# Performance work log

Measured on AMD Instinct MI355X. Metric: run time of the kernel, lower is better.

Reference implementation:

```python
import jax, jax.numpy as jnp
import numpy as np

NUM_GRAPHS = 4
N_NODES = 50000
N_EDGES = 800000
D_IN = 64
D_HID = 64
D_OUT = 64


def setup_inputs() -> dict:
    key = jax.random.key(0)
    ks = jax.random.split(key, 8)
    x = jax.random.normal(ks[0], (NUM_GRAPHS, N_NODES, D_IN), dtype=jnp.float32)
    edge_index = jax.random.randint(ks[1], (NUM_GRAPHS, 2, N_EDGES), 0, N_NODES, dtype=jnp.int64)
    s = 0.05
    W_l1 = jax.random.normal(ks[2], (NUM_GRAPHS, D_IN, D_HID), dtype=jnp.float32) * s
    W_r1 = jax.random.normal(ks[3], (NUM_GRAPHS, D_IN, D_HID), dtype=jnp.float32) * s
    b1 = jax.random.normal(ks[4], (NUM_GRAPHS, D_HID), dtype=jnp.float32) * s
    W_l2 = jax.random.normal(ks[5], (NUM_GRAPHS, D_HID, D_OUT), dtype=jnp.float32) * s
    W_r2 = jax.random.normal(ks[6], (NUM_GRAPHS, D_HID, D_OUT), dtype=jnp.float32) * s
    b2 = jax.random.normal(ks[7], (NUM_GRAPHS, D_OUT), dtype=jnp.float32) * s
    return {"x": x, "edge_index": edge_index, "W_l1": W_l1, "W_r1": W_r1,
            "b1": b1, "W_l2": W_l2, "W_r2": W_r2, "b2": b2}


def _sage_conv(x, src, dst, W_l, W_r, b):
    # PyG SAGEConv (aggr='mean', root_weight=True): mean(x[src] -> dst) @ W_l + b + x @ W_r
    n = x.shape[0]
    msgs = x[src]                                            # [E, d] irregular gather
    agg = jax.ops.segment_sum(msgs, dst, num_segments=n)     # [N, d]
    deg = jax.ops.segment_sum(jnp.ones((src.shape[0],), x.dtype), dst, num_segments=n)
    mean = agg / jnp.maximum(deg, 1.0)[:, None]              # empty neighborhoods -> 0
    return mean @ W_l + b + x @ W_r


def _per_graph(x, edge_index, W_l1, W_r1, b1, W_l2, W_r2, b2):
    src, dst = edge_index[0], edge_index[1]
    h = jax.nn.elu(_sage_conv(x, src, dst, W_l1, W_r1, b1))
    return jax.nn.elu(_sage_conv(h, src, dst, W_l2, W_r2, b2))


def reference(x, edge_index, W_l1, W_r1, b1, W_l2, W_r2, b2):
    out = jax.vmap(_per_graph)(x, edge_index, W_l1, W_r1, b1, W_l2, W_r2, b2)  # [G, N, out]
    return out.reshape(-1, out.shape[-1])  # concat along node dim -> [G*N, out]
```

## Files before the change

kernel.cpp:

```cpp
#include <hip/hip_runtime.h>
#include <hip/hip_bf16.h>
#include <math.h>

#define NG 4
#define NN 50000
#define NE 800000
#define DD 64
#define CAP 64
#define NT 64
#define NTILE 391
#define NTG (2 * NTILE)
#define RCAP 1536
#define CPAD 16
#define PBLK 128
#define CHUNK (NE / PBLK)
#define LBINS 392
#define BCAP 20

typedef __attribute__((ext_vector_type(8))) short short8;
typedef __attribute__((ext_vector_type(4))) float float4v;

__device__ __forceinline__ unsigned short f2b(float f) {
    union { __hip_bfloat16 h; unsigned short u; } cv;
    cv.h = __float2bfloat16(f);
    return cv.u;
}
__device__ __forceinline__ float b2f(unsigned short u) {
    union { unsigned short u; __hip_bfloat16 h; } cv;
    cv.u = u;
    return __bfloat162float(cv.h);
}

__global__ void init_kernel(const int* __restrict__ ei, int* __restrict__ flags) {
    __shared__ alignas(16) unsigned short A[16 * 32];
    __shared__ unsigned short B[32 * 16];
    int t = threadIdx.x;
    int any_nonzero = 0;
    for (int i = t; i < 128; i += 64) any_nonzero |= ei[2 * i + 1];
    unsigned long long nz = __ballot(any_nonzero != 0);
    int is64 = (nz == 0ULL) ? 1 : 0;
    for (int i = t; i < 512; i += 64) {
        int r = i >> 5, k = i & 31;
        A[i] = f2b((float)(((r * 5 + k * 3) & 31) - 15));
        int kk = i >> 4, c = i & 15;
        B[i] = f2b((float)(((kk * 7 + c * 11) & 31) - 15));
    }
    __syncthreads();
    short8 a = *(const short8*)&A[(t & 15) * 32 + (t >> 4) * 8];
    int c = t & 15, kb = (t >> 4) * 8;
    short8 b;
    for (int j = 0; j < 8; ++j) b[j] = (short)B[(kb + j) * 16 + c];
    float4v acc = {0.f, 0.f, 0.f, 0.f};
    acc = __builtin_amdgcn_mfma_f32_16x16x32_bf16(a, b, acc, 0, 0, 0);
    int ok = 1;
    for (int reg = 0; reg < 4; ++reg) {
        int row = (t >> 4) * 4 + reg;
        float ref = 0.f;
        for (int k = 0; k < 32; ++k)
            ref += (float)(((row * 5 + k * 3) & 31) - 15) *
                   (float)(((k * 7 + c * 11) & 31) - 15);
        if (acc[reg] != ref) ok = 0;
    }
    unsigned long long vote = __ballot(ok);
    if (t == 0) flags[0] = is64 | ((vote == ~0ULL) ? 2 : 0);
}

__device__ __forceinline__ int nt_idx(const int* __restrict__ ei, long pos, int is64) {
    return is64 ? __builtin_nontemporal_load(ei + 2 * pos)
                : __builtin_nontemporal_load(ei + pos);
}

__global__ void partition_kernel(const int* __restrict__ ei, const int* __restrict__ flags,
                                 int* __restrict__ bcnt, unsigned int* __restrict__ part) {
    __shared__ int lcnt[LBINS];
    __shared__ int basev[LBINS];
    __shared__ unsigned int lbuf[LBINS * BCAP];

    int is64 = flags[0] & 1;
    int s = blockIdx.x & 7;
    int g = s >> 1;
    int lo = (s & 1) * (NN / 2), hi = lo + (NN / 2);
    int rbase0 = lo >> 6;
    int bsl = blockIdx.x >> 3;
    int e0 = bsl * CHUNK, e1 = e0 + CHUNK;
    long ebase = (long)g * 2 * NE;

    for (int i = threadIdx.x; i < LBINS; i += 256) lcnt[i] = 0;
    __syncthreads();

    for (int e = e0 + threadIdx.x; e < e1; e += 256) {
        int d = nt_idx(ei, ebase + NE + e, is64);
        int sc = nt_idx(ei, ebase + e, is64);
        if (d >= lo && d < hi) {
            int lb = (d >> 6) - rbase0;
            unsigned int pk = ((unsigned int)d << 16) | (unsigned int)(sc & 0xffff);
            int pos = atomicAdd(&lcnt[lb], 1);
            if (pos < BCAP) {
                lbuf[lb * BCAP + pos] = pk;
            } else {
                int gp = atomicAdd(&bcnt[(g * NTG + (d >> 6)) * CPAD], 1);
                if (gp < RCAP) part[(long)(g * NTG + (d >> 6)) * RCAP + gp] = pk;
            }
        }
    }
    __syncthreads();

    for (int r = threadIdx.x; r < LBINS; r += 256) {
        int c = lcnt[r]; c = c < BCAP ? c : BCAP;
        basev[r] = c ? atomicAdd(&bcnt[(g * NTG + rbase0 + r) * CPAD], c) : 0;
    }
    __syncthreads();

    int w = threadIdx.x >> 6, hw = (threadIdx.x >> 5) & 1, l32 = threadIdx.x & 31;
    for (int r = w * 2 + hw; r < LBINS; r += 8) {
        int c = lcnt[r]; c = c < BCAP ? c : BCAP;
        int b = basev[r];
        if (l32 < c && b + l32 < RCAP)
            part[(long)(g * NTG + rbase0 + r) * RCAP + b + l32] = lbuf[r * BCAP + l32];
    }
}

__global__ void convert_kernel(const float* __restrict__ x, unsigned short* __restrict__ xb) {
    long total = (long)NG * NN * DD / 4;
    long stride = (long)gridDim.x * blockDim.x;
    const float4* src = (const float4*)x;
    unsigned long long* dst = (unsigned long long*)xb;
    for (long i = (long)blockIdx.x * blockDim.x + threadIdx.x; i < total; i += stride) {
        float4 v = src[i];
        unsigned long long p = (unsigned long long)f2b(v.x)
                             | ((unsigned long long)f2b(v.y) << 16)
                             | ((unsigned long long)f2b(v.z) << 32)
                             | ((unsigned long long)f2b(v.w) << 48);
        dst[i] = p;
    }
}

__global__ void wconv_kernel(const float* __restrict__ Wl1, const float* __restrict__ Wr1,
                             const float* __restrict__ Wl2, const float* __restrict__ Wr2,
                             unsigned short* __restrict__ wsw) {
    int g = blockIdx.x & 3, layer = blockIdx.x >> 2;
    const float* Wl = layer ? Wl2 : Wl1;
    const float* Wr = layer ? Wr2 : Wr1;
    for (int i = threadIdx.x; i < 2 * DD * DD; i += 256) {
        int m = i >> 12, rem = i & 4095, k = rem >> 6, col = rem & 63;
        float wv = (m == 0 ? Wl : Wr)[(long)g * DD * DD + rem];
        wsw[(((long)layer * NG + g) * 2 + m) * DD * DD + col * DD + (k ^ ((col & 7) << 3))]
            = f2b(wv);
    }
}

template <int LAYER>
__launch_bounds__(256, 6)
__global__ void sage_mfma_kernel(const unsigned short* __restrict__ xin,
                                 const int* __restrict__ bcnt,
                                 const unsigned int* __restrict__ part,
                                 const unsigned short* __restrict__ wsw,
                                 const float* __restrict__ bias, void* __restrict__ outp,
                                 const int* __restrict__ flags) {
    if (!(flags[0] & 2)) return;
    __shared__ alignas(16) unsigned short sWT[2 * DD * DD];
    __shared__ alignas(16) unsigned short sM[NT * DD];
    __shared__ int cnt_lds[NT];

    int s = blockIdx.x & 7, tb = blockIdx.x >> 3;
    int g = s >> 1;
    int tile = (s & 1) * NTILE + tb;
    int base = tile * NT;
    long gn0 = (long)g * NN;

    if (threadIdx.x < NT) cnt_lds[threadIdx.x] = 0;

    {
        const short8* wsrc = (const short8*)(wsw + ((long)LAYER * NG + g) * 2 * DD * DD);
        short8* wdst = (short8*)sWT;
        for (int i = threadIdx.x; i < 1024; i += 256) wdst[i] = wsrc[i];
    }
    __syncthreads();

    int rc = bcnt[(g * NTG + tile) * CPAD];
    int rcount = rc < RCAP ? rc : RCAP;
    const unsigned int* reg = part + (long)(g * NTG + tile) * RCAP;
    for (int i = threadIdx.x; i < rcount; i += 256) {
        unsigned int p = __builtin_nontemporal_load(reg + i);
        int dl = (p >> 16) & 63;
        int pos = atomicAdd(&cnt_lds[dl], 1);
        if (pos < CAP) sM[dl * DD + pos] = (unsigned short)(p & 0xffffu);
    }
    __syncthreads();

    int lane = threadIdx.x & 63;
    int w = threadIdx.x >> 6;
    int grp = lane >> 4;
    int fq  = lane & 15;
    const char* xg = (const char*)xin + (gn0 << 7);

#pragma unroll 1
    for (int j = 0; j < 8; ++j) {
        int rA = w * 16 + j, rB = rA + 8;
        int neA = cnt_lds[rA], neB = cnt_lds[rB];
        int nuA = neA < CAP ? neA : CAP; if (base + rA >= NN) nuA = 0;
        int nuB = neB < CAP ? neB : CAP; if (base + rB >= NN) nuB = 0;
        int msA = (int)sM[rA * DD + lane];
        int msB = (int)sM[rB * DD + lane];
        float a0 = 0.f, a1 = 0.f, a2 = 0.f, a3 = 0.f;
        float b0 = 0.f, b1 = 0.f, b2 = 0.f, b3 = 0.f;
        int numax = nuA > nuB ? nuA : nuB;
#pragma unroll 4
        for (int e = 0; e < numax; e += 4) {
            int ei = e + grp;
            bool vA = ei < nuA, vB = ei < nuB;
            int sA = __shfl(msA, vA ? ei : 0);
            int sB = __shfl(msB, vB ? ei : 0);
            sA = sA < NN - 1 ? sA : NN - 1;
            sB = sB < NN - 1 ? sB : NN - 1;
            unsigned long long va =
                *(const unsigned long long*)(xg + ((long)sA << 7) + (fq << 3));
            unsigned long long vb =
                *(const unsigned long long*)(xg + ((long)sB << 7) + (fq << 3));
            unsigned int ua0 = (unsigned int)va, ua1 = (unsigned int)(va >> 32);
            unsigned int ub0 = (unsigned int)vb, ub1 = (unsigned int)(vb >> 32);
            if (!vA) { ua0 = 0u; ua1 = 0u; }
            if (!vB) { ub0 = 0u; ub1 = 0u; }
            a0 += __uint_as_float(ua0 << 16);
            a1 += __uint_as_float(ua0 & 0xffff0000u);
            a2 += __uint_as_float(ua1 << 16);
            a3 += __uint_as_float(ua1 & 0xffff0000u);
            b0 += __uint_as_float(ub0 << 16);
            b1 += __uint_as_float(ub0 & 0xffff0000u);
            b2 += __uint_as_float(ub1 << 16);
            b3 += __uint_as_float(ub1 & 0xffff0000u);
        }
        a0 += __shfl_xor(a0, 16); a0 += __shfl_xor(a0, 32);
        a1 += __shfl_xor(a1, 16); a1 += __shfl_xor(a1, 32);
        a2 += __shfl_xor(a2, 16); a2 += __shfl_xor(a2, 32);
        a3 += __shfl_xor(a3, 16); a3 += __shfl_xor(a3, 32);
        b0 += __shfl_xor(b0, 16); b0 += __shfl_xor(b0, 32);
        b1 += __shfl_xor(b1, 16); b1 += __shfl_xor(b1, 32);
        b2 += __shfl_xor(b2, 16); b2 += __shfl_xor(b2, 32);
        b3 += __shfl_xor(b3, 16); b3 += __shfl_xor(b3, 32);
        float invA = 1.f / fmaxf((float)neA, 1.f);
        float invB = 1.f / fmaxf((float)neB, 1.f);
        a0 *= invA; a1 *= invA; a2 *= invA; a3 *= invA;
        b0 *= invB; b1 *= invB; b2 *= invB; b3 *= invB;
        unsigned long long pA =
            (unsigned long long)((unsigned int)f2b(a0) | ((unsigned int)f2b(a1) << 16))
            | ((unsigned long long)((unsigned int)f2b(a2) | ((unsigned int)f2b(a3) << 16)) << 32);
        unsigned long long pB =
            (unsigned long long)((unsigned int)f2b(b0) | ((unsigned int)f2b(b1) << 16))
            | ((unsigned long long)((unsigned int)f2b(b2) | ((unsigned int)f2b(b3) << 16)) << 32);
        if (grp == 0) {
            int swz = (fq * 4) ^ ((rA & 7) << 3);
            *(unsigned long long*)&sM[rA * DD + swz] = pA;
        } else if (grp == 1) {
            int swz = (fq * 4) ^ ((rB & 7) << 3);
            *(unsigned long long*)&sM[rB * DD + swz] = pB;
        }
    }

    int arow = w * 16 + (lane & 15);
    int kb = (lane >> 4) * 8;
    int selfrow = base + arow; if (selfrow > NN - 1) selfrow = NN - 1;
    short8 am[2], ax[2];
#pragma unroll
    for (int ss = 0; ss < 2; ++ss) {
        int f0 = (kb + 32 * ss) ^ ((arow & 7) << 3);
        am[ss] = *(const short8*)&sM[arow * DD + f0];
        ax[ss] = *(const short8*)&xin[(gn0 + selfrow) * DD + kb + 32 * ss];
    }

    float4v acc[4];
#pragma unroll
    for (int c = 0; c < 4; ++c) {
        float b = bias[g * DD + c * 16 + (lane & 15)];
        acc[c] = {b, b, b, b};
    }
#pragma unroll
    for (int c = 0; c < 4; ++c) {
        int col = c * 16 + (lane & 15);
        int cswz = (col & 7) << 3;
#pragma unroll
        for (int ss = 0; ss < 2; ++ss) {
            short8 bl = *(const short8*)&sWT[0 * DD * DD + col * DD + ((kb + 32 * ss) ^ cswz)];
            acc[c] = __builtin_amdgcn_mfma_f32_16x16x32_bf16(am[ss], bl, acc[c], 0, 0, 0);
        }
#pragma unroll
        for (int ss = 0; ss < 2; ++ss) {
            short8 br = *(const short8*)&sWT[1 * DD * DD + col * DD + ((kb + 32 * ss) ^ cswz)];
            acc[c] = __builtin_amdgcn_mfma_f32_16x16x32_bf16(ax[ss], br, acc[c], 0, 0, 0);
        }
    }

    int q = lane >> 4, cl = lane & 15;
#pragma unroll
    for (int c = 0; c < 4; ++c) {
        int col = c * 16 + cl;
#pragma unroll
        for (int r = 0; r < 4; ++r) {
            int grow = base + w * 16 + q * 4 + r;
            if (grow >= NN) continue;
            float v = acc[c][r];
            v = v > 0.f ? v : expm1f(v);
            if (LAYER == 0)
                ((unsigned short*)outp)[(gn0 + grow) * DD + col] = f2b(v);
            else
                __builtin_nontemporal_store(v, &((float*)outp)[(gn0 + grow) * DD + col]);
        }
    }
}

template <int LAYER>
__global__ void fallback_kernel(const unsigned short* __restrict__ xin,
                                const int* __restrict__ bcnt,
                                const unsigned int* __restrict__ part,
                                const float* __restrict__ Wl, const float* __restrict__ Wr,
                                const float* __restrict__ bias, void* __restrict__ outp,
                                const int* __restrict__ flags) {
    if (flags[0] & 2) return;
    __shared__ float sWl[DD * DD];
    __shared__ float sWr[DD * DD];
    __shared__ float sb[DD];
    __shared__ unsigned short bk[NT * CAP];
    __shared__ int cnt_lds[NT];

    int s = blockIdx.x & 7, tb = blockIdx.x >> 3;
    int g = s >> 1;
    int tile = (s & 1) * NTILE + tb;
    int base = tile * NT;
    long gn0 = (long)g * NN;

    if (threadIdx.x < NT) cnt_lds[threadIdx.x] = 0;
    for (int i = threadIdx.x; i < DD * DD; i += blockDim.x) {
        sWl[i] = Wl[(long)g * DD * DD + i];
        sWr[i] = Wr[(long)g * DD * DD + i];
    }
    if (threadIdx.x < DD) sb[threadIdx.x] = bias[g * DD + threadIdx.x];
    __syncthreads();

    int rc = bcnt[(g * NTG + tile) * CPAD];
    int rcount = rc < RCAP ? rc : RCAP;
    const unsigned int* reg = part + (long)(g * NTG + tile) * RCAP;
    for (int i = threadIdx.x; i < rcount; i += 256) {
        unsigned int p = reg[i];
        int dl = (p >> 16) & 63;
        int pos = atomicAdd(&cnt_lds[dl], 1);
        if (pos < CAP) bk[dl * CAP + pos] = (unsigned short)(p & 0xffffu);
    }
    __syncthreads();

    int lane = threadIdx.x & 63;
    int w = threadIdx.x >> 6;
    for (int j = 0; j < 16; ++j) {
        int rl = w * 16 + j;
        int node = base + rl;
        if (node >= NN) continue;
        long row = gn0 + node;
        int ne = cnt_lds[rl];
        int nuse = ne < CAP ? ne : CAP;
        int msrc = (int)bk[rl * CAP + lane];
        float sum = 0.f;
        for (int e = 0; e < nuse; ++e) {
            int a0 = __shfl(msrc, e);
            sum += b2f(xin[(gn0 + a0) * DD + lane]);
        }
        float mean = sum / fmaxf((float)ne, 1.f);
        float self = b2f(xin[row * DD + lane]);
        float acc = sb[lane];
#pragma unroll
        for (int k = 0; k < DD; ++k) {
            float mk = __shfl(mean, k);
            float xk = __shfl(self, k);
            acc += mk * sWl[k * DD + lane] + xk * sWr[k * DD + lane];
        }
        acc = acc > 0.f ? acc : expm1f(acc);
        if (LAYER == 0) ((unsigned short*)outp)[row * DD + lane] = f2b(acc);
        else            ((float*)outp)[row * DD + lane] = acc;
    }
}

extern "C" void kernel_launch(void* const* d_in, const int* in_sizes, int n_in,
                              void* d_out, int out_size, void* d_ws, size_t ws_size,
                              hipStream_t stream) {
    const float* x   = (const float*)d_in[0];
    const int*   ei  = (const int*)d_in[1];
    const float* Wl1 = (const float*)d_in[2];
    const float* Wr1 = (const float*)d_in[3];
    const float* b1  = (const float*)d_in[4];
    const float* Wl2 = (const float*)d_in[5];
    const float* Wr2 = (const float*)d_in[6];
    const float* b2  = (const float*)d_in[7];
    float* out = (float*)d_out;

    unsigned int* part = (unsigned int*)d_ws;
    int* bcnt = (int*)(part + (size_t)NG * NTG * RCAP);
    unsigned short* h = (unsigned short*)(bcnt + (size_t)NG * NTG * CPAD);
    unsigned short* wsw = h + (size_t)NG * NN * DD;
    int* flags = (int*)(wsw + (size_t)2 * NG * 2 * DD * DD);
    unsigned short* xb = (unsigned short*)d_out;

    hipMemsetAsync(bcnt, 0, (size_t)NG * NTG * CPAD * sizeof(int), stream);
    init_kernel<<<1, 64, 0, stream>>>(ei, flags);
    partition_kernel<<<PBLK * 8, 256, 0, stream>>>(ei, flags, bcnt, part);
    convert_kernel<<<2048, 256, 0, stream>>>(x, xb);
    wconv_kernel<<<8, 256, 0, stream>>>(Wl1, Wr1, Wl2, Wr2, wsw);

    const int grid = NTILE * 8;
    sage_mfma_kernel<0><<<grid, 256, 0, stream>>>(xb, bcnt, part, wsw, b1, h, flags);
    fallback_kernel<0><<<grid, 256, 0, stream>>>(xb, bcnt, part, Wl1, Wr1, b1, h, flags);
    sage_mfma_kernel<1><<<grid, 256, 0, stream>>>(h, bcnt, part, wsw, b2, out, flags);
    fallback_kernel<1><<<grid, 256, 0, stream>>>(h, bcnt, part, Wl2, Wr2, b2, out, flags);
}
```

Measured before the change: 267.0 us.

## Split neighbor gather into source-half phases for cache locality

Edges are partitioned per destination tile and also by which half of the source node range they come from. Each layer now runs two kernels: phase0 gathers from the low half and stores partial bf16 sums plus counts, and phase1 gathers from the high half, adds the partial, normalizes and does the MFMA transform. The aim is to shrink the working set of each gather pass so it stays in cache better. The cost is an extra kernel launch per layer, a round trip of the partial sums through global memory, and an extra bf16 rounding of the partial sums.

After: 340.5 us. 27.5% more time.

```diff
diff --git a/kernel.cpp b/kernel.cpp
--- a/kernel.cpp
+++ b/kernel.cpp
@@ -10,12 +10,12 @@
 #define NT 64
 #define NTILE 391
 #define NTG (2 * NTILE)
-#define RCAP 1536
+#define HCAP 768
 #define CPAD 16
 #define PBLK 128
 #define CHUNK (NE / PBLK)
 #define LBINS 392
-#define BCAP 20
+#define BCAP2 10
 
 typedef __attribute__((ext_vector_type(8))) short short8;
 typedef __attribute__((ext_vector_type(4))) float float4v;
@@ -72,9 +72,9 @@
 
 __global__ void partition_kernel(const int* __restrict__ ei, const int* __restrict__ flags,
                                  int* __restrict__ bcnt, unsigned int* __restrict__ part) {
-    __shared__ int lcnt[LBINS];
-    __shared__ int basev[LBINS];
-    __shared__ unsigned int lbuf[LBINS * BCAP];
+    __shared__ int lcnt[LBINS * 2];
+    __shared__ int basev[LBINS * 2];
+    __shared__ unsigned int lbuf[LBINS * 2 * BCAP2];
 
     int is64 = flags[0] & 1;
     int s = blockIdx.x & 7;
@@ -85,38 +85,42 @@
     int e0 = bsl * CHUNK, e1 = e0 + CHUNK;
     long ebase = (long)g * 2 * NE;
 
-    for (int i = threadIdx.x; i < LBINS; i += 256) lcnt[i] = 0;
+    for (int i = threadIdx.x; i < LBINS * 2; i += 256) lcnt[i] = 0;
     __syncthreads();
 
     for (int e = e0 + threadIdx.x; e < e1; e += 256) {
         int d = nt_idx(ei, ebase + NE + e, is64);
         int sc = nt_idx(ei, ebase + e, is64);
         if (d >= lo && d < hi) {
-            int lb = (d >> 6) - rbase0;
+            int hf = (sc >= NN / 2) ? 1 : 0;
+            int lb = ((d >> 6) - rbase0) * 2 + hf;
             unsigned int pk = ((unsigned int)d << 16) | (unsigned int)(sc & 0xffff);
             int pos = atomicAdd(&lcnt[lb], 1);
-            if (pos < BCAP) {
-                lbuf[lb * BCAP + pos] = pk;
+            if (pos < BCAP2) {
+                lbuf[lb * BCAP2 + pos] = pk;
             } else {
-                int gp = atomicAdd(&bcnt[(g * NTG + (d >> 6)) * CPAD], 1);
-                if (gp < RCAP) part[(long)(g * NTG + (d >> 6)) * RCAP + gp] = pk;
+                int pidx = (g * NTG + (d >> 6)) * 2 + hf;
+                int gp = atomicAdd(&bcnt[pidx * CPAD], 1);
+                if (gp < HCAP) part[(long)pidx * HCAP + gp] = pk;
             }
         }
     }
     __syncthreads();
 
-    for (int r = threadIdx.x; r < LBINS; r += 256) {
-        int c = lcnt[r]; c = c < BCAP ? c : BCAP;
-        basev[r] = c ? atomicAdd(&bcnt[(g * NTG + rbase0 + r) * CPAD], c) : 0;
+    for (int r = threadIdx.x; r < LBINS * 2; r += 256) {
+        int c = lcnt[r]; c = c < BCAP2 ? c : BCAP2;
+        int pidx = (g * NTG + rbase0 + (r >> 1)) * 2 + (r & 1);
+        basev[r] = c ? atomicAdd(&bcnt[pidx * CPAD], c) : 0;
     }
     __syncthreads();
 
     int w = threadIdx.x >> 6, hw = (threadIdx.x >> 5) & 1, l32 = threadIdx.x & 31;
-    for (int r = w * 2 + hw; r < LBINS; r += 8) {
-        int c = lcnt[r]; c = c < BCAP ? c : BCAP;
+    for (int r = w * 2 + hw; r < LBINS * 2; r += 8) {
+        int c = lcnt[r]; c = c < BCAP2 ? c : BCAP2;
         int b = basev[r];
-        if (l32 < c && b + l32 < RCAP)
-            part[(long)(g * NTG + rbase0 + r) * RCAP + b + l32] = lbuf[r * BCAP + l32];
+        int pidx = (g * NTG + rbase0 + (r >> 1)) * 2 + (r & 1);
+        if (l32 < c && b + l32 < HCAP)
+            part[(long)pidx * HCAP + b + l32] = lbuf[r * BCAP2 + l32];
     }
 }
 
@@ -149,16 +153,15 @@
     }
 }
 
-template <int LAYER>
-__launch_bounds__(256, 6)
-__global__ void sage_mfma_kernel(const unsigned short* __restrict__ xin,
-                                 const int* __restrict__ bcnt,
-                                 const unsigned int* __restrict__ part,
-                                 const unsigned short* __restrict__ wsw,
-                                 const float* __restrict__ bias, void* __restrict__ outp,
-                                 const int* __restrict__ flags) {
+template <int PSHIFT>
+__launch_bounds__(256, 8)
+__global__ void sage_phase0_kernel(const unsigned short* __restrict__ xin,
+                                   const int* __restrict__ bcnt,
+                                   const unsigned int* __restrict__ part,
+                                   unsigned short* __restrict__ cnt0,
+                                   char* __restrict__ ppart,
+                                   const int* __restrict__ flags) {
     if (!(flags[0] & 2)) return;
-    __shared__ alignas(16) unsigned short sWT[2 * DD * DD];
     __shared__ alignas(16) unsigned short sM[NT * DD];
     __shared__ int cnt_lds[NT];
 
@@ -169,18 +172,12 @@
     long gn0 = (long)g * NN;
 
     if (threadIdx.x < NT) cnt_lds[threadIdx.x] = 0;
-
-    {
-        const short8* wsrc = (const short8*)(wsw + ((long)LAYER * NG + g) * 2 * DD * DD);
-        short8* wdst = (short8*)sWT;
-        for (int i = threadIdx.x; i < 1024; i += 256) wdst[i] = wsrc[i];
-    }
-    __syncthreads();
-
-    int rc = bcnt[(g * NTG + tile) * CPAD];
-    int rcount = rc < RCAP ? rc : RCAP;
-    const unsigned int* reg = part + (long)(g * NTG + tile) * RCAP;
-    for (int i = threadIdx.x; i < rcount; i += 256) {
+    __syncthreads();
+
+    int pidx = (g * NTG + tile) * 2 + 0;
+    int rc = bcnt[pidx * CPAD]; rc = rc < HCAP ? rc : HCAP;
+    const unsigned int* reg = part + (long)pidx * HCAP;
+    for (int i = threadIdx.x; i < rc; i += 256) {
         unsigned int p = __builtin_nontemporal_load(reg + i);
         int dl = (p >> 16) & 63;
         int pos = atomicAdd(&cnt_lds[dl], 1);
@@ -188,10 +185,14 @@
     }
     __syncthreads();
 
+    if (threadIdx.x < NT) {
+        int node = base + threadIdx.x;
+        if (node < NN) cnt0[gn0 + node] = (unsigned short)cnt_lds[threadIdx.x];
+    }
+
     int lane = threadIdx.x & 63;
     int w = threadIdx.x >> 6;
-    int grp = lane >> 4;
-    int fq  = lane & 15;
+    int grp = lane >> 4, fq = lane & 15;
     const char* xg = (const char*)xin + (gn0 << 7);
 
 #pragma unroll 1
@@ -205,7 +206,7 @@
         float a0 = 0.f, a1 = 0.f, a2 = 0.f, a3 = 0.f;
         float b0 = 0.f, b1 = 0.f, b2 = 0.f, b3 = 0.f;
         int numax = nuA > nuB ? nuA : nuB;
-#pragma unroll 4
+#pragma unroll 2
         for (int e = 0; e < numax; e += 4) {
             int ei = e + grp;
             bool vA = ei < nuA, vB = ei < nuB;
@@ -238,20 +239,145 @@
         b1 += __shfl_xor(b1, 16); b1 += __shfl_xor(b1, 32);
         b2 += __shfl_xor(b2, 16); b2 += __shfl_xor(b2, 32);
         b3 += __shfl_xor(b3, 16); b3 += __shfl_xor(b3, 32);
-        float invA = 1.f / fmaxf((float)neA, 1.f);
-        float invB = 1.f / fmaxf((float)neB, 1.f);
-        a0 *= invA; a1 *= invA; a2 *= invA; a3 *= invA;
-        b0 *= invB; b1 *= invB; b2 *= invB; b3 *= invB;
         unsigned long long pA =
             (unsigned long long)((unsigned int)f2b(a0) | ((unsigned int)f2b(a1) << 16))
             | ((unsigned long long)((unsigned int)f2b(a2) | ((unsigned int)f2b(a3) << 16)) << 32);
         unsigned long long pB =
             (unsigned long long)((unsigned int)f2b(b0) | ((unsigned int)f2b(b1) << 16))
             | ((unsigned long long)((unsigned int)f2b(b2) | ((unsigned int)f2b(b3) << 16)) << 32);
+        if (grp == 0 && base + rA < NN)
+            *(unsigned long long*)(ppart + (((long)(gn0 + base + rA)) << PSHIFT) + (fq << 3)) = pA;
+        else if (grp == 1 && base + rB < NN)
+            *(unsigned long long*)(ppart + (((long)(gn0 + base + rB)) << PSHIFT) + (fq << 3)) = pB;
+    }
+}
+
+template <int LAYER>
+__launch_bounds__(256, 6)
+__global__ void sage_phase1_kernel(const unsigned short* __restrict__ xin,
+                                   const int* __restrict__ bcnt,
+                                   const unsigned int* __restrict__ part,
+                                   const unsigned short* __restrict__ cnt0,
+                                   const char* __restrict__ ppart,
+                                   const unsigned short* __restrict__ wsw,
+                                   const float* __restrict__ bias, void* __restrict__ outp,
+                                   const int* __restrict__ flags) {
+    if (!(flags[0] & 2)) return;
+    __shared__ alignas(16) unsigned short sWT[2 * DD * DD];
+    __shared__ alignas(16) unsigned short sM[NT * DD];
+    __shared__ int cnt_lds[NT];
+    const int PSHIFT = LAYER ? 8 : 7;
+
+    int s = blockIdx.x & 7, tb = blockIdx.x >> 3;
+    int g = s >> 1;
+    int tile = (s & 1) * NTILE + tb;
+    int base = tile * NT;
+    long gn0 = (long)g * NN;
+
+    if (threadIdx.x < NT) cnt_lds[threadIdx.x] = 0;
+
+    {
+        const short8* wsrc = (const short8*)(wsw + ((long)LAYER * NG + g) * 2 * DD * DD);
+        short8* wdst = (short8*)sWT;
+        for (int i = threadIdx.x; i < 1024; i += 256) wdst[i] = wsrc[i];
+    }
+    __syncthreads();
+
+    int pidx = (g * NTG + tile) * 2 + 1;
+    int rc = bcnt[pidx * CPAD]; rc = rc < HCAP ? rc : HCAP;
+    const unsigned int* reg = part + (long)pidx * HCAP;
+    for (int i = threadIdx.x; i < rc; i += 256) {
+        unsigned int p = __builtin_nontemporal_load(reg + i);
+        int dl = (p >> 16) & 63;
+        int pos = atomicAdd(&cnt_lds[dl], 1);
+        if (pos < CAP) sM[dl * DD + pos] = (unsigned short)((p & 0xffffu) | 0x0u);
+    }
+    __syncthreads();
+
+    int lane = threadIdx.x & 63;
+    int w = threadIdx.x >> 6;
+    int grp = lane >> 4, fq = lane & 15;
+    const char* xg = (const char*)xin + (gn0 << 7);
+
+#pragma unroll 1
+    for (int j = 0; j < 8; ++j) {
+        int rA = w * 16 + j, rB = rA + 8;
+        int nodeA = base + rA, nodeB = base + rB;
+        int ne1A = cnt_lds[rA], ne1B = cnt_lds[rB];
+        int ne0A = nodeA < NN ? (int)cnt0[gn0 + nodeA] : 0;
+        int ne0B = nodeB < NN ? (int)cnt0[gn0 + nodeB] : 0;
+        int nuA = ne1A < CAP ? ne1A : CAP; if (nodeA >= NN) nuA = 0;
+        int nuB = ne1B < CAP ? ne1B : CAP; if (nodeB >= NN) nuB = 0;
+        int msA = (int)sM[rA * DD + lane];
+        int msB = (int)sM[rB * DD + lane];
+        float a0 = 0.f, a1 = 0.f, a2 = 0.f, a3 = 0.f;
+        float b0 = 0.f, b1 = 0.f, b2 = 0.f, b3 = 0.f;
+        int numax = nuA > nuB ? nuA : nuB;
+#pragma unroll 2
+        for (int e = 0; e < numax; e += 4) {
+            int ei = e + grp;
+            bool vA = ei < nuA, vB = ei < nuB;
+            int sA = __shfl(msA, vA ? ei : 0);
+            int sB = __shfl(msB, vB ? ei : 0);
+            sA = sA < NN - 1 ? sA : NN - 1;
+            sB = sB < NN - 1 ? sB : NN - 1;
+            unsigned long long va =
+                *(const unsigned long long*)(xg + ((long)sA << 7) + (fq << 3));
+            unsigned long long vb =
+                *(const unsigned long long*)(xg + ((long)sB << 7) + (fq << 3));
+            unsigned int ua0 = (unsigned int)va, ua1 = (unsigned int)(va >> 32);
+            unsigned int ub0 = (unsigned int)vb, ub1 = (unsigned int)(vb >> 32);
+            if (!vA) { ua0 = 0u; ua1 = 0u; }
+            if (!vB) { ub0 = 0u; ub1 = 0u; }
+            a0 += __uint_as_float(ua0 << 16);
+            a1 += __uint_as_float(ua0 & 0xffff0000u);
+            a2 += __uint_as_float(ua1 << 16);
+            a3 += __uint_as_float(ua1 & 0xffff0000u);
+            b0 += __uint_as_float(ub0 << 16);
+            b1 += __uint_as_float(ub0 & 0xffff0000u);
+            b2 += __uint_as_float(ub1 << 16);
+            b3 += __uint_as_float(ub1 & 0xffff0000u);
+        }
+        a0 += __shfl_xor(a0, 16); a0 += __shfl_xor(a0, 32);
+        a1 += __shfl_xor(a1, 16); a1 += __shfl_xor(a1, 32);
+        a2 += __shfl_xor(a2, 16); a2 += __shfl_xor(a2, 32);
+        a3 += __shfl_xor(a3, 16); a3 += __shfl_xor(a3, 32);
+        b0 += __shfl_xor(b0, 16); b0 += __shfl_xor(b0, 32);
+        b1 += __shfl_xor(b1, 16); b1 += __shfl_xor(b1, 32);
+        b2 += __shfl_xor(b2, 16); b2 += __shfl_xor(b2, 32);
+        b3 += __shfl_xor(b3, 16); b3 += __shfl_xor(b3, 32);
         if (grp == 0) {
+            if (nodeA < NN) {
+                unsigned long long q = *(const unsigned long long*)
+                    (ppart + (((long)(gn0 + nodeA)) << PSHIFT) + (fq << 3));
+                unsigned int q0 = (unsigned int)q, q1 = (unsigned int)(q >> 32);
+                a0 += __uint_as_float(q0 << 16);
+                a1 += __uint_as_float(q0 & 0xffff0000u);
+                a2 += __uint_as_float(q1 << 16);
+                a3 += __uint_as_float(q1 & 0xffff0000u);
+            }
+            float inv = 1.f / fmaxf((float)(ne0A + ne1A), 1.f);
+            a0 *= inv; a1 *= inv; a2 *= inv; a3 *= inv;
+            unsigned long long pA =
+                (unsigned long long)((unsigned int)f2b(a0) | ((unsigned int)f2b(a1) << 16))
+                | ((unsigned long long)((unsigned int)f2b(a2) | ((unsigned int)f2b(a3) << 16)) << 32);
             int swz = (fq * 4) ^ ((rA & 7) << 3);
             *(unsigned long long*)&sM[rA * DD + swz] = pA;
         } else if (grp == 1) {
+            if (nodeB < NN) {
+                unsigned long long q = *(const unsigned long long*)
+                    (ppart + (((long)(gn0 + nodeB)) << PSHIFT) + (fq << 3));
+                unsigned int q0 = (unsigned int)q, q1 = (unsigned int)(q >> 32);
+                b0 += __uint_as_float(q0 << 16);
+                b1 += __uint_as_float(q0 & 0xffff0000u);
+                b2 += __uint_as_float(q1 << 16);
+                b3 += __uint_as_float(q1 & 0xffff0000u);
+            }
+            float inv = 1.f / fmaxf((float)(ne0B + ne1B), 1.f);
+            b0 *= inv; b1 *= inv; b2 *= inv; b3 *= inv;
+            unsigned long long pB =
+                (unsigned long long)((unsigned int)f2b(b0) | ((unsigned int)f2b(b1) << 16))
+                | ((unsigned long long)((unsigned int)f2b(b2) | ((unsigned int)f2b(b3) << 16)) << 32);
             int swz = (fq * 4) ^ ((rB & 7) << 3);
             *(unsigned long long*)&sM[rB * DD + swz] = pB;
         }
@@ -336,14 +462,16 @@
     if (threadIdx.x < DD) sb[threadIdx.x] = bias[g * DD + threadIdx.x];
     __syncthreads();
 
-    int rc = bcnt[(g * NTG + tile) * CPAD];
-    int rcount = rc < RCAP ? rc : RCAP;
-    const unsigned int* reg = part + (long)(g * NTG + tile) * RCAP;
-    for (int i = threadIdx.x; i < rcount; i += 256) {
-        unsigned int p = reg[i];
-        int dl = (p >> 16) & 63;
-        int pos = atomicAdd(&cnt_lds[dl], 1);
-        if (pos < CAP) bk[dl * CAP + pos] = (unsigned short)(p & 0xffffu);
+    for (int hf = 0; hf < 2; ++hf) {
+        int pidx = (g * NTG + tile) * 2 + hf;
+        int rc = bcnt[pidx * CPAD]; rc = rc < HCAP ? rc : HCAP;
+        const unsigned int* reg = part + (long)pidx * HCAP;
+        for (int i = threadIdx.x; i < rc; i += 256) {
+            unsigned int p = reg[i];
+            int dl = (p >> 16) & 63;
+            int pos = atomicAdd(&cnt_lds[dl], 1);
+            if (pos < CAP) bk[dl * CAP + pos] = (unsigned short)(p & 0xffffu);
+        }
     }
     __syncthreads();
 
@@ -391,21 +519,26 @@
     float* out = (float*)d_out;
 
     unsigned int* part = (unsigned int*)d_ws;
-    int* bcnt = (int*)(part + (size_t)NG * NTG * RCAP);
-    unsigned short* h = (unsigned short*)(bcnt + (size_t)NG * NTG * CPAD);
+    int* bcnt = (int*)(part + (size_t)NG * NTG * 2 * HCAP);
+    unsigned short* h = (unsigned short*)(bcnt + (size_t)NG * NTG * 2 * CPAD);
     unsigned short* wsw = h + (size_t)NG * NN * DD;
-    int* flags = (int*)(wsw + (size_t)2 * NG * 2 * DD * DD);
+    unsigned short* cnt0 = wsw + (size_t)2 * NG * 2 * DD * DD;
+    int* flags = (int*)(cnt0 + (size_t)NG * NN);
     unsigned short* xb = (unsigned short*)d_out;
 
-    hipMemsetAsync(bcnt, 0, (size_t)NG * NTG * CPAD * sizeof(int), stream);
+    hipMemsetAsync(bcnt, 0, (size_t)NG * NTG * 2 * CPAD * sizeof(int), stream);
     init_kernel<<<1, 64, 0, stream>>>(ei, flags);
     partition_kernel<<<PBLK * 8, 256, 0, stream>>>(ei, flags, bcnt, part);
     convert_kernel<<<2048, 256, 0, stream>>>(x, xb);
     wconv_kernel<<<8, 256, 0, stream>>>(Wl1, Wr1, Wl2, Wr2, wsw);
 
     const int grid = NTILE * 8;
-    sage_mfma_kernel<0><<<grid, 256, 0, stream>>>(xb, bcnt, part, wsw, b1, h, flags);
+    sage_phase0_kernel<7><<<grid, 256, 0, stream>>>(xb, bcnt, part, cnt0, (char*)h, flags);
+    sage_phase1_kernel<0><<<grid, 256, 0, stream>>>(xb, bcnt, part, cnt0, (const char*)h,
+                                                    wsw, b1, h, flags);
     fallback_kernel<0><<<grid, 256, 0, stream>>>(xb, bcnt, part, Wl1, Wr1, b1, h, flags);
-    sage_mfma_kernel<1><<<grid, 256, 0, stream>>>(h, bcnt, part, wsw, b2, out, flags);
+    sage_phase0_kernel<8><<<grid, 256, 0, stream>>>(h, bcnt, part, cnt0, (char*)out, flags);
+    sage_phase1_kernel<1><<<grid, 256, 0, stream>>>(h, bcnt, part, cnt0, (const char*)out,
+                                                    wsw, b2, out, flags);
     fallback_kernel<1><<<grid, 256, 0, stream>>>(h, bcnt, part, Wl2, Wr2, b2, out, flags);
 }
```
